# Performance work log

Measured on AMD Instinct MI355X. Metric: run time of the kernel, lower is better.

Reference implementation:

```python
import jax, jax.numpy as jnp
import numpy as np

MAX_NEIGHBORS = 64  # static cap; >> observed max (~50) for n=9225 uniform pts, r=0.03


def setup_inputs() -> dict:
    key = jax.random.key(0)
    k1, k2 = jax.random.split(key)
    n_batch, n, m, d = 8, 9225, 4096, 2
    data = jax.random.uniform(k1, (n_batch, n, d), dtype=jnp.float32)
    queries = jax.random.uniform(k2, (n_batch, m, d), dtype=jnp.float32)
    radius = jnp.float32(0.03)
    return {"data": data, "queries": queries, "radius": radius}


def reference(data, queries, radius):
    # Faithful JAX translation of native_neighbor_search (use_open3d=False),
    # computed in one shot instead of q_chunk loops (same math), with a static
    # neighbor cap MAX_NEIGHBORS standing in for the data-dependent max.
    B, n, d = data.shape
    m = queries.shape[1]
    # Squared Euclidean distances via the GEMM expansion (equiv. to cdist<=r).
    qn = jnp.sum(queries * queries, axis=-1)              # [B, m]
    dn = jnp.sum(data * data, axis=-1)                    # [B, n]
    cross = jnp.einsum("bmd,bnd->bmn", queries, data)    # [B, m, n]
    sqd = jnp.maximum(qn[:, :, None] + dn[:, None, :] - 2.0 * cross, 0.0)
    in_nbr = sqd <= radius * radius                       # [B, m, n] bool
    counts = jnp.sum(in_nbr, axis=2).astype(jnp.int32)    # [B, m]
    idx = jnp.arange(n, dtype=jnp.int32)                  # [n]
    # invalid slots -> sentinel n, sort compacts valid indices to the front
    valid = jnp.where(in_nbr, idx[None, None, :], jnp.int32(n))
    sorted_idx = jnp.sort(valid, axis=2)[:, :, :MAX_NEIGHBORS]
    neighbors_index = jnp.where(sorted_idx == n, jnp.int32(-1), sorted_idx)
    neighbors_row_splits = jnp.concatenate(
        [jnp.zeros((B, 1), dtype=jnp.int32), jnp.cumsum(counts, axis=1)], axis=1
    )
    return neighbors_index, neighbors_row_splits
```

## Files before the change

### kernel.cpp

```cpp
#include <hip/hip_runtime.h>

#define BATCH 8
#define NPTS 9225
#define MQ 4096
#define CAP 64
#define GRID 64
#define NCELLS (GRID * GRID)

__device__ __forceinline__ int cell_of(float x, float y) {
  int cx = (int)(x * (float)GRID);
  int cy = (int)(y * (float)GRID);
  cx = min(max(cx, 0), GRID - 1);
  cy = min(max(cy, 0), GRID - 1);
  return cy * GRID + cx;
}

__global__ __launch_bounds__(1024) void build_kernel(
    const float* __restrict__ data,
    int* __restrict__ cell_starts,
    float4* __restrict__ recs) {
  __shared__ int hist[NCELLS];
  __shared__ int cursor[NCELLS];
  __shared__ int wavesum[16];
  const int b = blockIdx.x;
  const int t = threadIdx.x;
#pragma unroll
  for (int k = 0; k < NCELLS / 1024; ++k) hist[t + k * 1024] = 0;
  __syncthreads();

  const float2* dp = (const float2*)data + (size_t)b * NPTS;
  for (int i = t; i < NPTS; i += 1024)
    atomicAdd(&hist[cell_of(dp[i].x, dp[i].y)], 1);
  __syncthreads();

  const int c0 = hist[4 * t + 0], c1 = hist[4 * t + 1];
  const int c2 = hist[4 * t + 2], c3 = hist[4 * t + 3];
  const int s = c0 + c1 + c2 + c3;
  const int lane = t & 63, wid = t >> 6;
  int v = s;
#pragma unroll
  for (int off = 1; off < 64; off <<= 1) {
    const int u = __shfl_up(v, off, 64);
    if (lane >= off) v += u;
  }
  if (lane == 63) wavesum[wid] = v;
  __syncthreads();
  int woff = 0;
  for (int k = 0; k < wid; ++k) woff += wavesum[k];
  int e = woff + v - s;
  int* cs = cell_starts + b * (NCELLS + 1);
  cs[4 * t + 0] = e; cursor[4 * t + 0] = e; e += c0;
  cs[4 * t + 1] = e; cursor[4 * t + 1] = e; e += c1;
  cs[4 * t + 2] = e; cursor[4 * t + 2] = e; e += c2;
  cs[4 * t + 3] = e; cursor[4 * t + 3] = e; e += c3;
  if (t == 1023) cs[NCELLS] = e;
  __syncthreads();

  float4* rb = recs + (size_t)b * NPTS;
  for (int i = t; i < NPTS; i += 1024) {
    const float2 p = dp[i];
    const int pos = atomicAdd(&cursor[cell_of(p.x, p.y)], 1);
    rb[pos] = make_float4(p.x, p.y, __int_as_float(i), 0.0f);
  }
}

__global__ __launch_bounds__(1024) void search_kernel(
    const float* __restrict__ queries, const float* __restrict__ radius_p,
    const int* __restrict__ cell_starts, const float4* __restrict__ recs,
    int* __restrict__ nbr_idx, int* __restrict__ counts) {
#pragma clang fp contract(off)
  __shared__ int hitbuf[16][CAP];
  const int lane = threadIdx.x & 63;
  const int w = __builtin_amdgcn_readfirstlane(threadIdx.x >> 6);
  const int q = blockIdx.x * 16 + w;
  const int b = q >> 12;
  const float r = radius_p[0];
  const float r2 = r * r;
  const float2 qv = ((const float2*)queries)[q];
  const float qx = qv.x, qy = qv.y;
  const float qn = qx * qx + qy * qy;

  const int cx = __builtin_amdgcn_readfirstlane(
      min(max((int)(qx * (float)GRID), 0), GRID - 1));
  const int cy = __builtin_amdgcn_readfirstlane(
      min(max((int)(qy * (float)GRID), 0), GRID - 1));
  const int x0 = max(cx - 2, 0), x1 = min(cx + 2, GRID - 1);
  const int y0 = max(cy - 2, 0), y1 = min(cy + 2, GRID - 1);

  const int csbase = b * (NCELLS + 1);
  int rstart[5], rlen[5];
  int nr = 0;
  for (int y = y0; y <= y1; ++y) {
    const int s0 = cell_starts[csbase + y * GRID + x0];
    const int s1 = cell_starts[csbase + y * GRID + x1 + 1];
    rstart[nr] = s0;
    rlen[nr] = s1 - s0;
    ++nr;
  }
  for (int k = nr; k < 5; ++k) { rstart[k] = 0; rlen[k] = 0; }
  const int L0 = rlen[0];
  const int L1 = L0 + rlen[1];
  const int L2 = L1 + rlen[2];
  const int L3 = L2 + rlen[3];
  const int T = L3 + rlen[4];

  const unsigned long long below = (1ull << lane) - 1ull;
  const float4* rb = recs + (size_t)b * NPTS;
  int h = 0;

  for (int base = 0; base < T; base += 64) {
    const int p = base + lane;
    const bool act = (p < T);
    int i;
    if (p < L0)      i = rstart[0] + p;
    else if (p < L1) i = rstart[1] + (p - L0);
    else if (p < L2) i = rstart[2] + (p - L1);
    else if (p < L3) i = rstart[3] + (p - L2);
    else             i = rstart[4] + (p - L3);
    if (!act) i = 0;
    const float4 rec = rb[i];
    const float dx = rec.x, dy = rec.y;
    const int id = __float_as_int(rec.z);
    const float dn = dx * dx + dy * dy;
    const float cross = qx * dx + qy * dy;
    const float s = (qn + dn) - 2.0f * cross;
    const bool in = act && (s <= r2);
    const unsigned long long mask = __ballot(in);
    if (in) {
      const int pos = h + __popcll(mask & below);
      if (pos < CAP) hitbuf[w][pos] = id;
    }
    h += __popcll(mask);
  }

  int v = (lane < h && lane < CAP) ? hitbuf[w][lane] : 0x7fffffff;

#pragma unroll
  for (int k = 2; k <= 32; k <<= 1) {
#pragma unroll
    for (int j = k >> 1; j >= 1; j >>= 1) {
      const int other = __shfl_xor(v, j, 64);
      const bool keep_min = (((lane & k) == 0) == ((lane & j) == 0));
      v = keep_min ? min(v, other) : max(v, other);
    }
  }
  if (h > 32) {
#pragma unroll
    for (int j = 32; j >= 1; j >>= 1) {
      const int other = __shfl_xor(v, j, 64);
      const bool keep_min = ((lane & j) == 0);
      v = keep_min ? min(v, other) : max(v, other);
    }
  }

  nbr_idx[(size_t)q * CAP + lane] = (v == 0x7fffffff) ? -1 : v;
  if (lane == 0) counts[q] = h;
}

__global__ __launch_bounds__(256) void scan_kernel(const int* __restrict__ counts,
                                                   int* __restrict__ row_splits) {
  const int b = blockIdx.x;
  const int t = threadIdx.x;
  const int PER = MQ / 256;
  __shared__ int buf[MQ + MQ / 16];
  __shared__ int partial[256];
  const int* c = counts + b * MQ;
#pragma unroll
  for (int k = 0; k < PER; ++k) {
    const int i = t + 256 * k;
    buf[i + (i >> 4)] = c[i];
  }
  __syncthreads();
  int local[PER];
  int sum = 0;
#pragma unroll
  for (int k = 0; k < PER; ++k) {
    const int i = t * PER + k;
    local[k] = buf[i + (i >> 4)];
    sum += local[k];
  }
  partial[t] = sum;
  __syncthreads();
  for (int off = 1; off < 256; off <<= 1) {
    int u = (t >= off) ? partial[t - off] : 0;
    __syncthreads();
    partial[t] += u;
    __syncthreads();
  }
  const int excl = (t == 0) ? 0 : partial[t - 1];
  int* rs = row_splits + b * (MQ + 1);
  if (t == 0) rs[0] = 0;
  int run = excl;
#pragma unroll
  for (int k = 0; k < PER; ++k) { run += local[k]; rs[t * PER + k + 1] = run; }
}

extern "C" void kernel_launch(void* const* d_in, const int* in_sizes, int n_in,
                              void* d_out, int out_size, void* d_ws, size_t ws_size,
                              hipStream_t stream) {
  const float* data    = (const float*)d_in[0];
  const float* queries = (const float*)d_in[1];
  const float* radius  = (const float*)d_in[2];
  int* out        = (int*)d_out;
  int* nbr_idx    = out;
  int* row_splits = out + BATCH * MQ * CAP;

  int* counts      = (int*)d_ws;
  int* cell_starts = counts + BATCH * MQ;
  float4* recs     = (float4*)(cell_starts + BATCH * (NCELLS + 1));

  hipLaunchKernelGGL(build_kernel, dim3(BATCH), dim3(1024), 0, stream,
                     data, cell_starts, recs);
  hipLaunchKernelGGL(search_kernel, dim3(BATCH * MQ / 16), dim3(1024), 0, stream,
                     queries, radius, cell_starts, recs, nbr_idx, counts);
  hipLaunchKernelGGL(scan_kernel, dim3(BATCH), dim3(256), 0, stream,
                     counts, row_splits);
}
```

Before: 92.96 us.

## Bin queries into coarse cells and share LDS-staged candidates per wave

The build kernel now also bins queries into a 32x32 grid, using extra blocks that run alongside the data binning. Each search wave handles one query cell rather than one query. It stages the candidate records from the surrounding 6x6 data cells into LDS once and reuses them for every query in that cell, which cuts repeated global loads of the same candidates. In exchange, each query scans a larger candidate window (often two 64-wide passes instead of one). Work also becomes uneven across waves because query cells hold different numbers of queries, and queries within a wave are processed one after another.

New measurement: 93.90 us. About the same (+1.0%).

```diff
diff --git a/kernel.cpp b/kernel.cpp
--- a/kernel.cpp
+++ b/kernel.cpp
@@ -6,155 +6,224 @@
 #define CAP 64
 #define GRID 64
 #define NCELLS (GRID * GRID)
-
-__device__ __forceinline__ int cell_of(float x, float y) {
-  int cx = (int)(x * (float)GRID);
-  int cy = (int)(y * (float)GRID);
-  cx = min(max(cx, 0), GRID - 1);
-  cy = min(max(cy, 0), GRID - 1);
-  return cy * GRID + cx;
-}
+#define QG 32
+#define NQC (QG * QG)
+#define STAGE 192
 
 __global__ __launch_bounds__(1024) void build_kernel(
-    const float* __restrict__ data,
+    const float* __restrict__ data, const float* __restrict__ queries,
     int* __restrict__ cell_starts,
-    float4* __restrict__ recs) {
+    float4* __restrict__ recs,
+    int* __restrict__ qcell_starts,
+    float4* __restrict__ qrecs) {
   __shared__ int hist[NCELLS];
   __shared__ int cursor[NCELLS];
   __shared__ int wavesum[16];
-  const int b = blockIdx.x;
   const int t = threadIdx.x;
-#pragma unroll
-  for (int k = 0; k < NCELLS / 1024; ++k) hist[t + k * 1024] = 0;
-  __syncthreads();
-
-  const float2* dp = (const float2*)data + (size_t)b * NPTS;
-  for (int i = t; i < NPTS; i += 1024)
-    atomicAdd(&hist[cell_of(dp[i].x, dp[i].y)], 1);
-  __syncthreads();
-
-  const int c0 = hist[4 * t + 0], c1 = hist[4 * t + 1];
-  const int c2 = hist[4 * t + 2], c3 = hist[4 * t + 3];
-  const int s = c0 + c1 + c2 + c3;
   const int lane = t & 63, wid = t >> 6;
-  int v = s;
-#pragma unroll
-  for (int off = 1; off < 64; off <<= 1) {
-    const int u = __shfl_up(v, off, 64);
-    if (lane >= off) v += u;
-  }
-  if (lane == 63) wavesum[wid] = v;
-  __syncthreads();
-  int woff = 0;
-  for (int k = 0; k < wid; ++k) woff += wavesum[k];
-  int e = woff + v - s;
-  int* cs = cell_starts + b * (NCELLS + 1);
-  cs[4 * t + 0] = e; cursor[4 * t + 0] = e; e += c0;
-  cs[4 * t + 1] = e; cursor[4 * t + 1] = e; e += c1;
-  cs[4 * t + 2] = e; cursor[4 * t + 2] = e; e += c2;
-  cs[4 * t + 3] = e; cursor[4 * t + 3] = e; e += c3;
-  if (t == 1023) cs[NCELLS] = e;
-  __syncthreads();
-
-  float4* rb = recs + (size_t)b * NPTS;
-  for (int i = t; i < NPTS; i += 1024) {
-    const float2 p = dp[i];
-    const int pos = atomicAdd(&cursor[cell_of(p.x, p.y)], 1);
-    rb[pos] = make_float4(p.x, p.y, __int_as_float(i), 0.0f);
-  }
-}
-
-__global__ __launch_bounds__(1024) void search_kernel(
-    const float* __restrict__ queries, const float* __restrict__ radius_p,
+
+  if (blockIdx.x < BATCH) {
+    const int b = blockIdx.x;
+#pragma unroll
+    for (int k = 0; k < NCELLS / 1024; ++k) hist[t + k * 1024] = 0;
+    __syncthreads();
+    const float2* dp = (const float2*)data + (size_t)b * NPTS;
+    for (int i = t; i < NPTS; i += 1024) {
+      const float2 p = dp[i];
+      const int cx = min(max((int)(p.x * (float)GRID), 0), GRID - 1);
+      const int cy = min(max((int)(p.y * (float)GRID), 0), GRID - 1);
+      atomicAdd(&hist[cy * GRID + cx], 1);
+    }
+    __syncthreads();
+    const int c0 = hist[4 * t + 0], c1 = hist[4 * t + 1];
+    const int c2 = hist[4 * t + 2], c3 = hist[4 * t + 3];
+    const int s = c0 + c1 + c2 + c3;
+    int v = s;
+#pragma unroll
+    for (int off = 1; off < 64; off <<= 1) {
+      const int u = __shfl_up(v, off, 64);
+      if (lane >= off) v += u;
+    }
+    if (lane == 63) wavesum[wid] = v;
+    __syncthreads();
+    int woff = 0;
+    for (int k = 0; k < wid; ++k) woff += wavesum[k];
+    int e = woff + v - s;
+    int* cs = cell_starts + b * (NCELLS + 1);
+    cs[4 * t + 0] = e; cursor[4 * t + 0] = e; e += c0;
+    cs[4 * t + 1] = e; cursor[4 * t + 1] = e; e += c1;
+    cs[4 * t + 2] = e; cursor[4 * t + 2] = e; e += c2;
+    cs[4 * t + 3] = e; cursor[4 * t + 3] = e; e += c3;
+    if (t == 1023) cs[NCELLS] = e;
+    __syncthreads();
+    float4* rb = recs + (size_t)b * NPTS;
+    for (int i = t; i < NPTS; i += 1024) {
+      const float2 p = dp[i];
+      const int cx = min(max((int)(p.x * (float)GRID), 0), GRID - 1);
+      const int cy = min(max((int)(p.y * (float)GRID), 0), GRID - 1);
+      const int pos = atomicAdd(&cursor[cy * GRID + cx], 1);
+      rb[pos] = make_float4(p.x, p.y, __int_as_float(i), 0.0f);
+    }
+  } else {
+    const int b = blockIdx.x - BATCH;
+    hist[t] = 0;
+    __syncthreads();
+    const float2* qp = (const float2*)queries + (size_t)b * MQ;
+#pragma unroll
+    for (int k = 0; k < MQ / 1024; ++k) {
+      const float2 p = qp[t + k * 1024];
+      const int cx = min(max((int)(p.x * (float)QG), 0), QG - 1);
+      const int cy = min(max((int)(p.y * (float)QG), 0), QG - 1);
+      atomicAdd(&hist[cy * QG + cx], 1);
+    }
+    __syncthreads();
+    const int cval = hist[t];
+    int v = cval;
+#pragma unroll
+    for (int off = 1; off < 64; off <<= 1) {
+      const int u = __shfl_up(v, off, 64);
+      if (lane >= off) v += u;
+    }
+    if (lane == 63) wavesum[wid] = v;
+    __syncthreads();
+    int woff = 0;
+    for (int k = 0; k < wid; ++k) woff += wavesum[k];
+    const int excl = woff + v - cval;
+    int* cs = qcell_starts + b * (NQC + 1);
+    cs[t] = excl;
+    cursor[t] = excl;
+    if (t == NQC - 1) cs[NQC] = excl + cval;
+    __syncthreads();
+    float4* qr = qrecs + (size_t)b * MQ;
+#pragma unroll
+    for (int k = 0; k < MQ / 1024; ++k) {
+      const int i = t + k * 1024;
+      const float2 p = qp[i];
+      const int cx = min(max((int)(p.x * (float)QG), 0), QG - 1);
+      const int cy = min(max((int)(p.y * (float)QG), 0), QG - 1);
+      const int pos = atomicAdd(&cursor[cy * QG + cx], 1);
+      qr[pos] = make_float4(p.x, p.y, __int_as_float(i), 0.0f);
+    }
+  }
+}
+
+__global__ __launch_bounds__(256) void search_kernel(
+    const float* __restrict__ radius_p,
     const int* __restrict__ cell_starts, const float4* __restrict__ recs,
+    const int* __restrict__ qcell_starts, const float4* __restrict__ qrecs,
     int* __restrict__ nbr_idx, int* __restrict__ counts) {
 #pragma clang fp contract(off)
-  __shared__ int hitbuf[16][CAP];
+  __shared__ float4 stagebuf[4][STAGE];
+  __shared__ int hitbuf[4][CAP];
   const int lane = threadIdx.x & 63;
-  const int w = __builtin_amdgcn_readfirstlane(threadIdx.x >> 6);
-  const int q = blockIdx.x * 16 + w;
-  const int b = q >> 12;
+  const int w = threadIdx.x >> 6;
+  const int gw = blockIdx.x * 4 + w;
+  const int b = gw >> 10;
+  const int qc = gw & (NQC - 1);
+  const int qs = qcell_starts[b * (NQC + 1) + qc];
+  const int qe = qcell_starts[b * (NQC + 1) + qc + 1];
+  if (qs == qe) return;
+
+  const int qcx = qc & (QG - 1), qcy = qc >> 5;
+  const int x0 = max(2 * qcx - 2, 0), x1 = min(2 * qcx + 3, GRID - 1);
+  const int y0 = max(2 * qcy - 2, 0), y1 = min(2 * qcy + 3, GRID - 1);
+  const int csbase = b * (NCELLS + 1);
+  int rs[6], rl[6];
+#pragma unroll
+  for (int i = 0; i < 6; ++i) {
+    const int y = y0 + i;
+    if (y <= y1) {
+      rs[i] = cell_starts[csbase + y * GRID + x0];
+      rl[i] = cell_starts[csbase + y * GRID + x1 + 1] - rs[i];
+    } else {
+      rs[i] = 0; rl[i] = 0;
+    }
+  }
+  const int L0 = rl[0];
+  const int L1 = L0 + rl[1];
+  const int L2 = L1 + rl[2];
+  const int L3 = L2 + rl[3];
+  const int L4 = L3 + rl[4];
+  const int T = L4 + rl[5];
+
+  const float4* rb = recs + (size_t)b * NPTS;
+  for (int base = 0; base < T && base < STAGE; base += 64) {
+    const int p = base + lane;
+    int i;
+    if (p < L0)      i = rs[0] + p;
+    else if (p < L1) i = rs[1] + (p - L0);
+    else if (p < L2) i = rs[2] + (p - L1);
+    else if (p < L3) i = rs[3] + (p - L2);
+    else if (p < L4) i = rs[4] + (p - L3);
+    else             i = rs[5] + (p - L4);
+    if (p >= T) i = 0;
+    stagebuf[w][p] = rb[i];
+  }
+
+  const unsigned long long below = (1ull << lane) - 1ull;
   const float r = radius_p[0];
   const float r2 = r * r;
-  const float2 qv = ((const float2*)queries)[q];
-  const float qx = qv.x, qy = qv.y;
-  const float qn = qx * qx + qy * qy;
-
-  const int cx = __builtin_amdgcn_readfirstlane(
-      min(max((int)(qx * (float)GRID), 0), GRID - 1));
-  const int cy = __builtin_amdgcn_readfirstlane(
-      min(max((int)(qy * (float)GRID), 0), GRID - 1));
-  const int x0 = max(cx - 2, 0), x1 = min(cx + 2, GRID - 1);
-  const int y0 = max(cy - 2, 0), y1 = min(cy + 2, GRID - 1);
-
-  const int csbase = b * (NCELLS + 1);
-  int rstart[5], rlen[5];
-  int nr = 0;
-  for (int y = y0; y <= y1; ++y) {
-    const int s0 = cell_starts[csbase + y * GRID + x0];
-    const int s1 = cell_starts[csbase + y * GRID + x1 + 1];
-    rstart[nr] = s0;
-    rlen[nr] = s1 - s0;
-    ++nr;
-  }
-  for (int k = nr; k < 5; ++k) { rstart[k] = 0; rlen[k] = 0; }
-  const int L0 = rlen[0];
-  const int L1 = L0 + rlen[1];
-  const int L2 = L1 + rlen[2];
-  const int L3 = L2 + rlen[3];
-  const int T = L3 + rlen[4];
-
-  const unsigned long long below = (1ull << lane) - 1ull;
-  const float4* rb = recs + (size_t)b * NPTS;
-  int h = 0;
-
-  for (int base = 0; base < T; base += 64) {
-    const int p = base + lane;
-    const bool act = (p < T);
-    int i;
-    if (p < L0)      i = rstart[0] + p;
-    else if (p < L1) i = rstart[1] + (p - L0);
-    else if (p < L2) i = rstart[2] + (p - L1);
-    else if (p < L3) i = rstart[3] + (p - L2);
-    else             i = rstart[4] + (p - L3);
-    if (!act) i = 0;
-    const float4 rec = rb[i];
-    const float dx = rec.x, dy = rec.y;
-    const int id = __float_as_int(rec.z);
-    const float dn = dx * dx + dy * dy;
-    const float cross = qx * dx + qy * dy;
-    const float s = (qn + dn) - 2.0f * cross;
-    const bool in = act && (s <= r2);
-    const unsigned long long mask = __ballot(in);
-    if (in) {
-      const int pos = h + __popcll(mask & below);
-      if (pos < CAP) hitbuf[w][pos] = id;
-    }
-    h += __popcll(mask);
-  }
-
-  int v = (lane < h && lane < CAP) ? hitbuf[w][lane] : 0x7fffffff;
-
-#pragma unroll
-  for (int k = 2; k <= 32; k <<= 1) {
-#pragma unroll
-    for (int j = k >> 1; j >= 1; j >>= 1) {
-      const int other = __shfl_xor(v, j, 64);
-      const bool keep_min = (((lane & k) == 0) == ((lane & j) == 0));
-      v = keep_min ? min(v, other) : max(v, other);
-    }
-  }
-  if (h > 32) {
-#pragma unroll
-    for (int j = 32; j >= 1; j >>= 1) {
-      const int other = __shfl_xor(v, j, 64);
-      const bool keep_min = ((lane & j) == 0);
-      v = keep_min ? min(v, other) : max(v, other);
-    }
-  }
-
-  nbr_idx[(size_t)q * CAP + lane] = (v == 0x7fffffff) ? -1 : v;
-  if (lane == 0) counts[q] = h;
+
+  for (int k = qs; k < qe; ++k) {
+    const float4 qr = qrecs[(size_t)b * MQ + k];
+    const float qx = qr.x, qy = qr.y;
+    const int qid = __float_as_int(qr.z);
+    const float qn = qx * qx + qy * qy;
+    int h = 0;
+    for (int base = 0; base < T; base += 64) {
+      const int p = base + lane;
+      const bool act = (p < T);
+      float4 rec;
+      if (base < STAGE) {
+        rec = stagebuf[w][p];
+      } else {
+        int i;
+        if (p < L0)      i = rs[0] + p;
+        else if (p < L1) i = rs[1] + (p - L0);
+        else if (p < L2) i = rs[2] + (p - L1);
+        else if (p < L3) i = rs[3] + (p - L2);
+        else if (p < L4) i = rs[4] + (p - L3);
+        else             i = rs[5] + (p - L4);
+        if (!act) i = 0;
+        rec = rb[i];
+      }
+      const float dx = rec.x, dy = rec.y;
+      const int id = __float_as_int(rec.z);
+      const float dn = dx * dx + dy * dy;
+      const float cross = qx * dx + qy * dy;
+      const float s = (qn + dn) - 2.0f * cross;
+      const bool in = act && (s <= r2);
+      const unsigned long long mask = __ballot(in);
+      if (in) {
+        const int pos = h + __popcll(mask & below);
+        if (pos < CAP) hitbuf[w][pos] = id;
+      }
+      h += __popcll(mask);
+    }
+
+    int v = (lane < h && lane < CAP) ? hitbuf[w][lane] : 0x7fffffff;
+#pragma unroll
+    for (int kk = 2; kk <= 32; kk <<= 1) {
+#pragma unroll
+      for (int j = kk >> 1; j >= 1; j >>= 1) {
+        const int other = __shfl_xor(v, j, 64);
+        const bool keep_min = (((lane & kk) == 0) == ((lane & j) == 0));
+        v = keep_min ? min(v, other) : max(v, other);
+      }
+    }
+    if (h > 32) {
+#pragma unroll
+      for (int j = 32; j >= 1; j >>= 1) {
+        const int other = __shfl_xor(v, j, 64);
+        const bool keep_min = ((lane & j) == 0);
+        v = keep_min ? min(v, other) : max(v, other);
+      }
+    }
+
+    const int qglob = b * MQ + qid;
+    nbr_idx[(size_t)qglob * CAP + lane] = (v == 0x7fffffff) ? -1 : v;
+    if (lane == 0) counts[qglob] = h;
+  }
 }
 
 __global__ __launch_bounds__(256) void scan_kernel(const int* __restrict__ counts,
@@ -205,14 +274,17 @@
   int* nbr_idx    = out;
   int* row_splits = out + BATCH * MQ * CAP;
 
-  int* counts      = (int*)d_ws;
-  int* cell_starts = counts + BATCH * MQ;
-  float4* recs     = (float4*)(cell_starts + BATCH * (NCELLS + 1));
-
-  hipLaunchKernelGGL(build_kernel, dim3(BATCH), dim3(1024), 0, stream,
-                     data, cell_starts, recs);
-  hipLaunchKernelGGL(search_kernel, dim3(BATCH * MQ / 16), dim3(1024), 0, stream,
-                     queries, radius, cell_starts, recs, nbr_idx, counts);
+  int* counts       = (int*)d_ws;
+  int* cell_starts  = counts + BATCH * MQ;
+  int* qcell_starts = cell_starts + BATCH * (NCELLS + 1);
+  float4* recs      = (float4*)(qcell_starts + BATCH * (NQC + 1));
+  float4* qrecs     = recs + (size_t)BATCH * NPTS;
+
+  hipLaunchKernelGGL(build_kernel, dim3(2 * BATCH), dim3(1024), 0, stream,
+                     data, queries, cell_starts, recs, qcell_starts, qrecs);
+  hipLaunchKernelGGL(search_kernel, dim3(BATCH * NQC / 4), dim3(256), 0, stream,
+                     radius, cell_starts, recs, qcell_starts, qrecs,
+                     nbr_idx, counts);
   hipLaunchKernelGGL(scan_kernel, dim3(BATCH), dim3(256), 0, stream,
                      counts, row_splits);
 }
```
